# Optimization experiments

Measured on AMD Instinct MI355X. Metric: run time of the kernel, lower is better.

Reference implementation:

```python
import jax, jax.numpy as jnp
import numpy as np

E = 8
DIMS = [512, 1024, 1024, 512]
BATCH = 2048


def _init_w(key, shape):
    a = np.sqrt(6.0 / (shape[-2] * shape[-1]))
    return jax.random.uniform(key, shape, dtype=jnp.float32, minval=-a, maxval=a)


def setup_inputs() -> dict:
    key = jax.random.key(0)
    ks = jax.random.split(key, 8)
    inp = {
        "weight_blend": jax.random.uniform(ks[0], (BATCH, E), dtype=jnp.float32),
        "x": jax.random.normal(ks[1], (BATCH, DIMS[0]), dtype=jnp.float32),
    }
    for i in range(3):
        inp[f"W{i}"] = _init_w(ks[2 + i], (E, DIMS[i + 1], DIMS[i]))
        inp[f"B{i}"] = jnp.zeros((E, DIMS[i + 1], 1), dtype=jnp.float32)
    return inp


def reference(weight_blend, x, W0, B0, W1, B1, W2, B2):
    Ws = [W0, W1, W2]
    Bs = [B0, B1, B2]
    acts = [jax.nn.elu, jax.nn.elu, None]
    for W, B, act in zip(Ws, Bs, acts):
        # dropout p=0 -> identity
        # blended-expert GEMM: sum_e wb[b,e] * (W[e] @ x[b]) == einsum
        t = jnp.einsum("be,eoi,bi->bo", weight_blend, W, x)
        bias = jnp.einsum("be,eo->bo", weight_blend, B[..., 0])
        x = t + bias
        if act is not None:
            x = act(x)
    return x
```

## Files before the change

### kernel.cpp

```cpp
#include <hip/hip_runtime.h>
#include <math.h>

typedef __attribute__((ext_vector_type(8))) short bf16x8;
typedef __attribute__((ext_vector_type(4))) float f32x4;

#define NEXP 8
#define BATCH 2048

__device__ __forceinline__ unsigned short f2bf(float f) {
    union { float f; unsigned u; } v; v.f = f;
    unsigned r = v.u + 0x7FFFu + ((v.u >> 16) & 1u);
    return (unsigned short)(r >> 16);
}

__device__ __forceinline__ float elu_fast(float v) {
    return v > 0.f ? v : (exp2f(v * 1.4426950408889634f) - 1.0f);
}

__device__ __forceinline__ void gl_lds(const char* g, char* l) {
    __builtin_amdgcn_global_load_lds(
        (const __attribute__((address_space(1))) void*)g,
        (__attribute__((address_space(3))) void*)l, 16, 0, 0);
}

__global__ __launch_bounds__(256) void pack_all(
    const float* __restrict__ W0, const float* __restrict__ W1,
    const float* __restrict__ W2, const float* __restrict__ x,
    unsigned short* __restrict__ W0p, unsigned short* __restrict__ W1p,
    unsigned short* __restrict__ W2p, unsigned short* __restrict__ x0p)
{
    __shared__ float T[128 * 36];
    const int bid = blockIdx.x, t = threadIdx.x;

    if (bid < 10240) {
        const float* W; unsigned short* out; int KB, Din, Dout, U, lin;
        if (bid < 2048)      { W = W0; out = W0p; KB = 16; Din = 512;  Dout = 1024; U = 4; lin = bid; }
        else if (bid < 6144) { W = W1; out = W1p; KB = 32; Din = 1024; Dout = 1024; U = 4; lin = bid - 2048; }
        else                 { W = W2; out = W2p; KB = 32; Din = 1024; Dout = 512;  U = 2; lin = bid - 6144; }
        const int e  = lin & 7;
        const int r  = lin >> 3;
        const int kb = r % KB;
        const int nb = r / KB;
        const int N0 = nb * 16 * U;
        const int K0 = kb * 32;
        for (int it = 0; it < U / 2; ++it) {
            const int idx = t + 256 * it;
            const int nl = idx >> 3, k4 = (idx & 7) * 4;
            float4 v = *(const float4*)(W + ((size_t)e * Dout + N0 + nl) * Din + K0 + k4);
            *(float4*)(T + nl * 36 + k4) = v;
        }
        __syncthreads();
        if (t < 64 * U) {
            const int u = t >> 6, l = t & 63;
            const float* p = T + (u * 16 + (l & 15)) * 36 + (l >> 4) * 8;
            bf16x8 h;
            #pragma unroll
            for (int j = 0; j < 8; ++j) h[j] = (short)f2bf(p[j]);
            *(bf16x8*)(out + (size_t)lin * (U * 512) + t * 8) = h;
        }
    } else {
        const int lin = bid - 10240;
        const int kb = lin & 15, mb = lin >> 4;
        for (int it = 0; it < 4; ++it) {
            const int idx = t + 256 * it;
            const int ml = idx >> 3, k4 = (idx & 7) * 4;
            float4 v = *(const float4*)(x + (size_t)(mb * 128 + ml) * 512 + kb * 32 + k4);
            *(float4*)(T + ml * 36 + k4) = v;
        }
        __syncthreads();
        #pragma unroll
        for (int it = 0; it < 2; ++it) {
            const int s = t + 256 * it;
            const int g = s >> 6, l = s & 63;
            const float* p = T + (g * 16 + (l & 15)) * 36 + (l >> 4) * 8;
            bf16x8 h;
            #pragma unroll
            for (int j = 0; j < 8; ++j) h[j] = (short)f2bf(p[j]);
            *(bf16x8*)(x0p + (size_t)lin * 4096 + s * 8) = h;
        }
    }
}

template<int UP>
__device__ __forceinline__ void moe_stage(
    char* smem, int bx, int by,
    const unsigned short* __restrict__ Xp,
    const unsigned short* __restrict__ Wp,
    const float* __restrict__ Bias,
    const float* __restrict__ WBl,
    unsigned short* __restrict__ Yout,
    int KB, int Dout, int KBn)
{
    constexpr int PSTR = 68;
    constexpr unsigned BUFB = 40 * 1024;

    const int tid  = threadIdx.x;
    const int wv   = tid >> 6;
    const int mh   = wv >> 2;
    const int ew   = wv & 3;
    const int l    = tid & 63;
    const int lh   = l >> 4;
    const int ll   = l & 15;
    const int e0   = 2 * ew;
    const int m0   = by * 128 + mh * 64;
    const int n0   = bx * 64;
    const int mb   = by;

    f32x4 acc0[4][4], acc1[4][4];
    #pragma unroll
    for (int t = 0; t < 4; ++t)
        #pragma unroll
        for (int u = 0; u < 4; ++u)
            #pragma unroll
            for (int i = 0; i < 4; ++i) { acc0[t][u][i] = 0.f; acc1[t][u][i] = 0.f; }

    const char* xc = (const char*)Xp;
    const char* wc = (const char*)Wp;
    const int fidbase = wv * 5;
    const char* gp[5]; unsigned kst[5];
    #pragma unroll
    for (int s = 0; s < 5; ++s) {
        const int fid = fidbase + s;
        if (fid < 8) {
            gp[s]  = xc + (unsigned)(mb * KB) * 8192u + (unsigned)fid * 1024u + l * 16u;
            kst[s] = 8192u;
        } else {
            const int idx = fid - 8;
            const int e   = 2 * (idx >> 3) + ((idx >> 2) & 1);
            const int u   = idx & 3;
            const int fn  = bx * 4 + u;
            const int nb  = fn / UP;
            const int uu  = fn % UP;
            gp[s]  = wc + (unsigned)((nb * KB * 8 + e) * UP + uu) * 1024u + l * 16u;
            kst[s] = UP * 8192u;
        }
    }

    auto STAGE = [&](int b, int kk) {
        char* lb = smem + (unsigned)b * BUFB + (unsigned)fidbase * 1024u;
        #pragma unroll
        for (int s = 0; s < 5; ++s)
            gl_lds(gp[s] + (unsigned)kk * kst[s], lb + s * 1024);
    };

    auto COMPUTE = [&](int b) {
        const char* sb = smem + (unsigned)b * BUFB;
        bf16x8 aR[4], b0R[4], b1R[4];
        #pragma unroll
        for (int t = 0; t < 4; ++t)
            aR[t] = *(const bf16x8*)(sb + (mh * 4 + t) * 1024 + l * 16);
        #pragma unroll
        for (int u = 0; u < 4; ++u) {
            b0R[u] = *(const bf16x8*)(sb + (8 + ew * 8 + u) * 1024 + l * 16);
            b1R[u] = *(const bf16x8*)(sb + (8 + ew * 8 + 4 + u) * 1024 + l * 16);
        }
        __builtin_amdgcn_s_setprio(1);
        #pragma unroll
        for (int u = 0; u < 4; ++u)
            #pragma unroll
            for (int t = 0; t < 4; ++t) {
                acc0[t][u] = __builtin_amdgcn_mfma_f32_16x16x32_bf16(aR[t], b0R[u], acc0[t][u], 0, 0, 0);
                acc1[t][u] = __builtin_amdgcn_mfma_f32_16x16x32_bf16(aR[t], b1R[u], acc1[t][u], 0, 0, 0);
            }
        __builtin_amdgcn_s_setprio(0);
    };

    STAGE(0, 0);
    __syncthreads();
    for (int kk = 0; kk < KB; ++kk) {
        if (kk + 1 < KB) STAGE((kk + 1) & 1, kk + 1);
        COMPUTE(kk & 1);
        __syncthreads();
    }

    float* epi = (float*)smem;
    float bi0[4], bi1[4];
    #pragma unroll
    for (int u = 0; u < 4; ++u) {
        const int n = n0 + u * 16 + ll;
        bi0[u] = Bias[(size_t)e0 * Dout + n];
        bi1[u] = Bias[(size_t)(e0 + 1) * Dout + n];
    }
    float2 wbp[4][4];
    #pragma unroll
    for (int t = 0; t < 4; ++t)
        #pragma unroll
        for (int r = 0; r < 4; ++r) {
            const int lm = 16 * t + 4 * lh + r;
            wbp[t][r] = ((const float2*)(WBl + (size_t)(m0 + lm) * NEXP))[ew];
        }

    float* pb = epi + ew * (64 * PSTR);
    #pragma unroll
    for (int h = 0; h < 2; ++h) {
        if (mh == h) {
            #pragma unroll
            for (int t = 0; t < 4; ++t)
                #pragma unroll
                for (int r = 0; r < 4; ++r) {
                    const int lm = 16 * t + 4 * lh + r;
                    #pragma unroll
                    for (int u = 0; u < 4; ++u)
                        pb[lm * PSTR + u * 16 + ll] =
                            wbp[t][r].x * (acc0[t][u][r] + bi0[u]) + wbp[t][r].y * (acc1[t][u][r] + bi1[u]);
                }
        }
        __syncthreads();
        {
            const int kbh = wv >> 2;
            const int g   = wv & 3;
            const int rb  = (g * 16 + ll) * PSTR + kbh * 32 + lh * 8;
            bf16x8 hx;
            #pragma unroll
            for (int j = 0; j < 8; ++j) {
                float v = epi[0 * 64 * PSTR + rb + j]
                        + epi[1 * 64 * PSTR + rb + j]
                        + epi[2 * 64 * PSTR + rb + j]
                        + epi[3 * 64 * PSTR + rb + j];
                v = elu_fast(v);
                hx[j] = (short)f2bf(v);
            }
            unsigned short* dst = Yout +
                ((size_t)(mb * KBn + bx * 2 + kbh) * 8 + h * 4 + g) * 512 + l * 8;
            *(bf16x8*)dst = hx;
        }
        if (h == 0) __syncthreads();
    }
}

template<int UP, int NU>
__device__ __forceinline__ void moe_body(
    float* lds_f, int bx, int by,
    const unsigned short* __restrict__ Xp,
    const unsigned short* __restrict__ Wp,
    const float* __restrict__ Bias,
    const float* __restrict__ WBl,
    void* __restrict__ Yout,
    int KB, int Dout, int KBn, int act, int packed_out)
{
    constexpr int PSTR = NU * 16 + 4;

    const int tid  = threadIdx.x;
    const int ew   = tid >> 6;
    const int l    = tid & 63;
    const int lh   = l >> 4;
    const int ll   = l & 15;
    const int e0   = 2 * ew;
    const int m0   = by * 64;
    const int n0   = bx * (NU * 16);
    const int mb   = by >> 1;
    const int half = by & 1;

    f32x4 acc0[4][NU], acc1[4][NU];
    #pragma unroll
    for (int t = 0; t < 4; ++t)
        #pragma unroll
        for (int u = 0; u < NU; ++u)
            #pragma unroll
            for (int i = 0; i < 4; ++i) { acc0[t][u][i] = 0.f; acc1[t][u][i] = 0.f; }

    unsigned aoff[4];
    #pragma unroll
    for (int t = 0; t < 4; ++t)
        aoff[t] = (unsigned)(mb * KB) * 8192u + (unsigned)(half * 4 + t) * 1024u + l * 16u;
    unsigned boff0[NU], boff1[NU];
    #pragma unroll
    for (int u = 0; u < NU; ++u) {
        const int fn = bx * NU + u;
        const int nb = fn / UP;
        const int uu = fn % UP;
        boff0[u] = (((unsigned)(nb * KB) * 8 + e0) * UP + uu) * 1024u + l * 16u;
        boff1[u] = boff0[u] + UP * 1024u;
    }
    const unsigned astr = 8192u;
    const unsigned bstr = UP * 8192u;
    const char* xc = (const char*)Xp;
    const char* wc = (const char*)Wp;

    bf16x8 aR[2][4], b0R[2][NU], b1R[2][NU];

    auto LOAD = [&](int s, int kk) {
        const unsigned ab = (unsigned)kk * astr;
        const unsigned bb = (unsigned)kk * bstr;
        #pragma unroll
        for (int t = 0; t < 4; ++t)
            aR[s][t] = *(const bf16x8*)(xc + aoff[t] + ab);
        #pragma unroll
        for (int u = 0; u < NU; ++u) {
            b0R[s][u] = *(const bf16x8*)(wc + boff0[u] + bb);
            b1R[s][u] = *(const bf16x8*)(wc + boff1[u] + bb);
        }
    };
    auto MF = [&](int s) {
        __builtin_amdgcn_s_setprio(1);
        #pragma unroll
        for (int u = 0; u < NU; ++u)
            #pragma unroll
            for (int t = 0; t < 4; ++t) {
                acc0[t][u] = __builtin_amdgcn_mfma_f32_16x16x32_bf16(aR[s][t], b0R[s][u], acc0[t][u], 0, 0, 0);
                acc1[t][u] = __builtin_amdgcn_mfma_f32_16x16x32_bf16(aR[s][t], b1R[s][u], acc1[t][u], 0, 0, 0);
            }
        __builtin_amdgcn_s_setprio(0);
    };

    LOAD(0, 0);
    for (int kk = 0; kk < KB; kk += 2) {
        if (kk + 1 < KB) LOAD(1, kk + 1);
        MF(0);
        if (kk + 2 < KB) LOAD(0, kk + 2);
        MF(1);
    }

    float bi0[NU], bi1[NU];
    #pragma unroll
    for (int u = 0; u < NU; ++u) {
        const int n = n0 + u * 16 + ll;
        bi0[u] = Bias[(size_t)e0 * Dout + n];
        bi1[u] = Bias[(size_t)(e0 + 1) * Dout + n];
    }
    float2 wbp[4][4];
    #pragma unroll
    for (int t = 0; t < 4; ++t)
        #pragma unroll
        for (int r = 0; r < 4; ++r) {
            const int lm = 16 * t + 4 * lh + r;
            wbp[t][r] = ((const float2*)(WBl + (size_t)(m0 + lm) * NEXP))[ew];
        }

    float* pb = lds_f + ew * (64 * PSTR);
    #pragma unroll
    for (int t = 0; t < 4; ++t)
        #pragma unroll
        for (int r = 0; r < 4; ++r) {
            const int lm = 16 * t + 4 * lh + r;
            #pragma unroll
            for (int u = 0; u < NU; ++u)
                pb[lm * PSTR + u * 16 + ll] =
                    wbp[t][r].x * (acc0[t][u][r] + bi0[u]) + wbp[t][r].y * (acc1[t][u][r] + bi1[u]);
        }
    __syncthreads();

    if (packed_out) {
        if constexpr (NU == 4) {
            #pragma unroll
            for (int it = 0; it < 2; ++it) {
                const int kbh = it;
                const int g   = tid >> 6;
                const int le  = tid & 63;
                const int lhh = le >> 4, lle = le & 15;
                const int rb  = (g * 16 + lle) * PSTR + kbh * 32 + lhh * 8;
                bf16x8 h;
                #pragma unroll
                for (int j = 0; j < 8; ++j) {
                    float v = lds_f[0 * 64 * PSTR + rb + j]
                            + lds_f[1 * 64 * PSTR + rb + j]
                            + lds_f[2 * 64 * PSTR + rb + j]
                            + lds_f[3 * 64 * PSTR + rb + j];
                    if (act) v = elu_fast(v);
                    h[j] = (short)f2bf(v);
                }
                unsigned short* dst = (unsigned short*)Yout +
                    ((size_t)(mb * KBn + bx * 2 + kbh) * 8 + half * 4 + g) * 512 + le * 8;
                *(bf16x8*)dst = h;
            }
        }
    } else {
        constexpr int F4R = NU * 4;
        #pragma unroll
        for (int it = 0; it < NU; ++it) {
            const int idx = tid + 256 * it;
            const int row = idx / F4R;
            const int c4  = (idx % F4R) * 4;
            const int rb  = row * PSTR + c4;
            float4 s  = *(const float4*)(lds_f + 0 * 64 * PSTR + rb);
            float4 q1 = *(const float4*)(lds_f + 1 * 64 * PSTR + rb);
            float4 q2 = *(const float4*)(lds_f + 2 * 64 * PSTR + rb);
            float4 q3 = *(const float4*)(lds_f + 3 * 64 * PSTR + rb);
            s.x += q1.x + q2.x + q3.x;
            s.y += q1.y + q2.y + q3.y;
            s.z += q1.z + q2.z + q3.z;
            s.w += q1.w + q2.w + q3.w;
            if (act) {
                s.x = elu_fast(s.x);
                s.y = elu_fast(s.y);
                s.z = elu_fast(s.z);
                s.w = elu_fast(s.w);
            }
            *(float4*)((float*)Yout + (size_t)(m0 + row) * Dout + n0 + c4) = s;
        }
    }
}

__device__ __forceinline__ void swz256(int& bx, int& by) {
    const int bid = blockIdx.x;
    const int xcd = bid & 7;
    const int loc = bid >> 3;
    bx = xcd * 2 + (loc & 1);
    by = loc >> 1;
}
__device__ __forceinline__ void swz_pair(int& bx, int& by) {
    const int bid = blockIdx.x;
    const int xcd = bid & 7;
    const int loc = bid >> 3;
    bx = xcd * 2 + (loc & 1);
    by = loc >> 1;
}

__global__ __launch_bounds__(512, 2) void moe_l0(
    const unsigned short* __restrict__ Xp, const unsigned short* __restrict__ Wp,
    const float* __restrict__ Bias, const float* __restrict__ WBl,
    unsigned short* __restrict__ Yout, int KB, int Dout, int KBn)
{
    __shared__ __align__(16) char smem[2 * 40 * 1024];
    int bx, by; swz256(bx, by);
    moe_stage<4>(smem, bx, by, Xp, Wp, Bias, WBl, Yout, KB, Dout, KBn);
}
__global__ __launch_bounds__(512, 2) void moe_l1(
    const unsigned short* __restrict__ Xp, const unsigned short* __restrict__ Wp,
    const float* __restrict__ Bias, const float* __restrict__ WBl,
    unsigned short* __restrict__ Yout, int KB, int Dout, int KBn)
{
    __shared__ __align__(16) char smem[2 * 40 * 1024];
    int bx, by; swz256(bx, by);
    moe_stage<4>(smem, bx, by, Xp, Wp, Bias, WBl, Yout, KB, Dout, KBn);
}
__global__ __launch_bounds__(256, 2) void moe_l2(
    const unsigned short* __restrict__ Xp, const unsigned short* __restrict__ Wp,
    const float* __restrict__ Bias, const float* __restrict__ WBl,
    void* __restrict__ Yout, int KB, int Dout, int KBn, int act, int packed_out)
{
    __shared__ __align__(16) float lds_f[4 * 64 * 36];
    int bx, by; swz_pair(bx, by);
    moe_body<2, 2>(lds_f, bx, by, Xp, Wp, Bias, WBl, Yout, KB, Dout, KBn, act, packed_out);
}

#define BM 64
#define BNF 64
#define BKF 16
#define PAD 4

__global__ __launch_bounds__(256) void moe_layer_f32(
    const float* __restrict__ X, const float* __restrict__ W,
    const float* __restrict__ Bias, const float* __restrict__ WB,
    float* __restrict__ Y, int Din, int Dout, int act)
{
    __shared__ float As[BKF][BM + PAD];
    __shared__ float Bs[BKF][BNF + PAD];
    const int tid = threadIdx.x;
    const int tm = tid >> 4, tn = tid & 15;
    const int m0 = blockIdx.y * BM, n0 = blockIdx.x * BNF;
    const int lr = tid >> 2, lc = (tid & 3) << 2;
    float acc[4][4] = {};
    const float* xrow  = X  + (size_t)(m0 + lr) * Din;
    const float* wbrow = WB + (size_t)(m0 + lr) * NEXP;
    const float* wrow0 = W  + (size_t)(n0 + lr) * Din;
    for (int e = 0; e < NEXP; ++e) {
        const float wbe = wbrow[e];
        const float* wrow = wrow0 + (size_t)e * Dout * Din;
        for (int k0 = 0; k0 < Din; k0 += BKF) {
            float4 av = *(const float4*)(xrow + k0 + lc);
            float4 bv = *(const float4*)(wrow + k0 + lc);
            __syncthreads();
            As[lc+0][lr] = av.x*wbe; As[lc+1][lr] = av.y*wbe;
            As[lc+2][lr] = av.z*wbe; As[lc+3][lr] = av.w*wbe;
            Bs[lc+0][lr] = bv.x; Bs[lc+1][lr] = bv.y;
            Bs[lc+2][lr] = bv.z; Bs[lc+3][lr] = bv.w;
            __syncthreads();
            #pragma unroll
            for (int k = 0; k < BKF; ++k) {
                float4 a = *(const float4*)&As[k][tm << 2];
                float4 b = *(const float4*)&Bs[k][tn << 2];
                acc[0][0]+=a.x*b.x; acc[0][1]+=a.x*b.y; acc[0][2]+=a.x*b.z; acc[0][3]+=a.x*b.w;
                acc[1][0]+=a.y*b.x; acc[1][1]+=a.y*b.y; acc[1][2]+=a.y*b.z; acc[1][3]+=a.y*b.w;
                acc[2][0]+=a.z*b.x; acc[2][1]+=a.z*b.y; acc[2][2]+=a.z*b.z; acc[2][3]+=a.z*b.w;
                acc[3][0]+=a.w*b.x; acc[3][1]+=a.w*b.y; acc[3][2]+=a.w*b.z; acc[3][3]+=a.w*b.w;
            }
        }
    }
    #pragma unroll
    for (int im = 0; im < 4; ++im) {
        const int m = m0 + (tm << 2) + im;
        const float* wbm = WB + (size_t)m * NEXP;
        float wv[NEXP];
        #pragma unroll
        for (int e = 0; e < NEXP; ++e) wv[e] = wbm[e];
        #pragma unroll
        for (int in = 0; in < 4; ++in) {
            const int n = n0 + (tn << 2) + in;
            float bsum = 0.f;
            #pragma unroll
            for (int e = 0; e < NEXP; ++e) bsum += wv[e] * Bias[(size_t)e * Dout + n];
            float v = acc[im][in] + bsum;
            if (act) v = v > 0.f ? v : expm1f(v);
            acc[im][in] = v;
        }
        float4 o = make_float4(acc[im][0], acc[im][1], acc[im][2], acc[im][3]);
        *(float4*)(Y + (size_t)m * Dout + n0 + (tn << 2)) = o;
    }
}

extern "C" void kernel_launch(void* const* d_in, const int* in_sizes, int n_in,
                              void* d_out, int out_size, void* d_ws, size_t ws_size,
                              hipStream_t stream)
{
    (void)in_sizes; (void)n_in; (void)out_size;
    const float* wb = (const float*)d_in[0];
    const float* x  = (const float*)d_in[1];
    const float* W0 = (const float*)d_in[2];
    const float* B0 = (const float*)d_in[3];
    const float* W1 = (const float*)d_in[4];
    const float* B1 = (const float*)d_in[5];
    const float* W2 = (const float*)d_in[6];
    const float* B2 = (const float*)d_in[7];
    float* out = (float*)d_out;

    const size_t NW0 = (size_t)8*1024*512, NW1 = (size_t)8*1024*1024, NW2 = (size_t)8*512*1024;
    const size_t NX0 = (size_t)BATCH*512, NX1 = (size_t)BATCH*1024;
    const size_t need = (NW0 + NW1 + NW2 + NX0 + 2 * NX1) * 2;

    if (ws_size >= need) {
        unsigned short* W0p = (unsigned short*)d_ws;
        unsigned short* W1p = W0p + NW0;
        unsigned short* W2p = W1p + NW1;
        unsigned short* x0p = W2p + NW2;
        unsigned short* x1p = x0p + NX0;
        unsigned short* x2p = x1p + NX1;
        pack_all<<<10496, 256, 0, stream>>>(W0, W1, W2, x, W0p, W1p, W2p, x0p);
        moe_l0<<<256, 512, 0, stream>>>(x0p, W0p, B0, wb, x1p, 16, 1024, 32);
        moe_l1<<<256, 512, 0, stream>>>(x1p, W1p, B1, wb, x2p, 32, 1024, 32);
        moe_l2<<<512, 256, 0, stream>>>(x2p, W2p, B2, wb, out, 32, 512,  0, 0, 0);
    } else {
        float* x1 = (float*)d_ws;
        float* x2 = x1 + (size_t)BATCH * 1024;
        moe_layer_f32<<<dim3(1024/BNF, BATCH/BM), 256, 0, stream>>>(x,  W0, B0, wb, x1, 512,  1024, 1);
        moe_layer_f32<<<dim3(1024/BNF, BATCH/BM), 256, 0, stream>>>(x1, W1, B1, wb, x2, 1024, 1024, 1);
        moe_layer_f32<<<dim3(512/BNF,  BATCH/BM), 256, 0, stream>>>(x2, W2, B2, wb, out, 1024, 512,  0);
    }
}
```

Before: 186.9 us.

## Stage layer-2 operands through LDS with async global-to-LDS double buffering

```diff
diff --git a/kernel.cpp b/kernel.cpp
--- a/kernel.cpp
+++ b/kernel.cpp
@@ -228,17 +228,18 @@
     }
 }
 
-template<int UP, int NU>
-__device__ __forceinline__ void moe_body(
-    float* lds_f, int bx, int by,
+__device__ __forceinline__ void moe_stage_l2(
+    char* smem, int bx, int by,
     const unsigned short* __restrict__ Xp,
     const unsigned short* __restrict__ Wp,
     const float* __restrict__ Bias,
     const float* __restrict__ WBl,
-    void* __restrict__ Yout,
-    int KB, int Dout, int KBn, int act, int packed_out)
-{
-    constexpr int PSTR = NU * 16 + 4;
+    float* __restrict__ Yout,
+    int KB, int Dout)
+{
+    constexpr int UP = 2;
+    constexpr int PSTR = 36;
+    constexpr unsigned BUFB = 20 * 1024;
 
     const int tid  = threadIdx.x;
     const int ew   = tid >> 6;
@@ -247,73 +248,81 @@
     const int ll   = l & 15;
     const int e0   = 2 * ew;
     const int m0   = by * 64;
-    const int n0   = bx * (NU * 16);
+    const int n0   = bx * 32;
     const int mb   = by >> 1;
     const int half = by & 1;
 
-    f32x4 acc0[4][NU], acc1[4][NU];
+    f32x4 acc0[4][2], acc1[4][2];
     #pragma unroll
     for (int t = 0; t < 4; ++t)
         #pragma unroll
-        for (int u = 0; u < NU; ++u)
+        for (int u = 0; u < 2; ++u)
             #pragma unroll
             for (int i = 0; i < 4; ++i) { acc0[t][u][i] = 0.f; acc1[t][u][i] = 0.f; }
 
-    unsigned aoff[4];
-    #pragma unroll
-    for (int t = 0; t < 4; ++t)
-        aoff[t] = (unsigned)(mb * KB) * 8192u + (unsigned)(half * 4 + t) * 1024u + l * 16u;
-    unsigned boff0[NU], boff1[NU];
-    #pragma unroll
-    for (int u = 0; u < NU; ++u) {
-        const int fn = bx * NU + u;
-        const int nb = fn / UP;
-        const int uu = fn % UP;
-        boff0[u] = (((unsigned)(nb * KB) * 8 + e0) * UP + uu) * 1024u + l * 16u;
-        boff1[u] = boff0[u] + UP * 1024u;
-    }
-    const unsigned astr = 8192u;
-    const unsigned bstr = UP * 8192u;
     const char* xc = (const char*)Xp;
     const char* wc = (const char*)Wp;
-
-    bf16x8 aR[2][4], b0R[2][NU], b1R[2][NU];
-
-    auto LOAD = [&](int s, int kk) {
-        const unsigned ab = (unsigned)kk * astr;
-        const unsigned bb = (unsigned)kk * bstr;
+    const int fidbase = ew * 5;
+    const char* gp[5]; unsigned kst[5];
+    #pragma unroll
+    for (int s = 0; s < 5; ++s) {
+        const int fid = fidbase + s;
+        if (fid < 4) {
+            gp[s]  = xc + (unsigned)(mb * KB) * 8192u + (unsigned)(half * 4 + fid) * 1024u + l * 16u;
+            kst[s] = 8192u;
+        } else {
+            const int idx = fid - 4;
+            const int e   = idx >> 1;
+            const int u   = idx & 1;
+            const int fn  = bx * 2 + u;
+            const int nb  = fn / UP;
+            const int uu  = fn % UP;
+            gp[s]  = wc + (unsigned)((nb * KB * 8 + e) * UP + uu) * 1024u + l * 16u;
+            kst[s] = UP * 8192u;
+        }
+    }
+
+    auto STAGE = [&](int b, int kk) {
+        char* lb = smem + (unsigned)b * BUFB + (unsigned)fidbase * 1024u;
+        #pragma unroll
+        for (int s = 0; s < 5; ++s)
+            gl_lds(gp[s] + (unsigned)kk * kst[s], lb + s * 1024);
+    };
+
+    auto COMPUTE = [&](int b) {
+        const char* sb = smem + (unsigned)b * BUFB;
+        bf16x8 aR[4], b0R[2], b1R[2];
         #pragma unroll
         for (int t = 0; t < 4; ++t)
-            aR[s][t] = *(const bf16x8*)(xc + aoff[t] + ab);
-        #pragma unroll
-        for (int u = 0; u < NU; ++u) {
-            b0R[s][u] = *(const bf16x8*)(wc + boff0[u] + bb);
-            b1R[s][u] = *(const bf16x8*)(wc + boff1[u] + bb);
-        }
-    };
-    auto MF = [&](int s) {
+            aR[t] = *(const bf16x8*)(sb + t * 1024 + l * 16);
+        #pragma unroll
+        for (int u = 0; u < 2; ++u) {
+            b0R[u] = *(const bf16x8*)(sb + (4 + e0 * 2 + u) * 1024 + l * 16);
+            b1R[u] = *(const bf16x8*)(sb + (4 + (e0 + 1) * 2 + u) * 1024 + l * 16);
+        }
         __builtin_amdgcn_s_setprio(1);
         #pragma unroll
-        for (int u = 0; u < NU; ++u)
+        for (int u = 0; u < 2; ++u)
             #pragma unroll
             for (int t = 0; t < 4; ++t) {
-                acc0[t][u] = __builtin_amdgcn_mfma_f32_16x16x32_bf16(aR[s][t], b0R[s][u], acc0[t][u], 0, 0, 0);
-                acc1[t][u] = __builtin_amdgcn_mfma_f32_16x16x32_bf16(aR[s][t], b1R[s][u], acc1[t][u], 0, 0, 0);
+                acc0[t][u] = __builtin_amdgcn_mfma_f32_16x16x32_bf16(aR[t], b0R[u], acc0[t][u], 0, 0, 0);
+                acc1[t][u] = __builtin_amdgcn_mfma_f32_16x16x32_bf16(aR[t], b1R[u], acc1[t][u], 0, 0, 0);
             }
         __builtin_amdgcn_s_setprio(0);
     };
 
-    LOAD(0, 0);
-    for (int kk = 0; kk < KB; kk += 2) {
-        if (kk + 1 < KB) LOAD(1, kk + 1);
-        MF(0);
-        if (kk + 2 < KB) LOAD(0, kk + 2);
-        MF(1);
-    }
-
-    float bi0[NU], bi1[NU];
-    #pragma unroll
-    for (int u = 0; u < NU; ++u) {
+    STAGE(0, 0);
+    __syncthreads();
+    for (int kk = 0; kk < KB; ++kk) {
+        if (kk + 1 < KB) STAGE((kk + 1) & 1, kk + 1);
+        COMPUTE(kk & 1);
+        __syncthreads();
+    }
+
+    float* epi = (float*)smem;
+    float bi0[2], bi1[2];
+    #pragma unroll
+    for (int u = 0; u < 2; ++u) {
         const int n = n0 + u * 16 + ll;
         bi0[u] = Bias[(size_t)e0 * Dout + n];
         bi1[u] = Bias[(size_t)(e0 + 1) * Dout + n];
@@ -327,67 +336,34 @@
             wbp[t][r] = ((const float2*)(WBl + (size_t)(m0 + lm) * NEXP))[ew];
         }
 
-    float* pb = lds_f + ew * (64 * PSTR);
+    float* pb = epi + ew * (64 * PSTR);
     #pragma unroll
     for (int t = 0; t < 4; ++t)
         #pragma unroll
         for (int r = 0; r < 4; ++r) {
             const int lm = 16 * t + 4 * lh + r;
             #pragma unroll
-            for (int u = 0; u < NU; ++u)
+            for (int u = 0; u < 2; ++u)
                 pb[lm * PSTR + u * 16 + ll] =
                     wbp[t][r].x * (acc0[t][u][r] + bi0[u]) + wbp[t][r].y * (acc1[t][u][r] + bi1[u]);
         }
     __syncthreads();
 
-    if (packed_out) {
-        if constexpr (NU == 4) {
-            #pragma unroll
-            for (int it = 0; it < 2; ++it) {
-                const int kbh = it;
-                const int g   = tid >> 6;
-                const int le  = tid & 63;
-                const int lhh = le >> 4, lle = le & 15;
-                const int rb  = (g * 16 + lle) * PSTR + kbh * 32 + lhh * 8;
-                bf16x8 h;
-                #pragma unroll
-                for (int j = 0; j < 8; ++j) {
-                    float v = lds_f[0 * 64 * PSTR + rb + j]
-                            + lds_f[1 * 64 * PSTR + rb + j]
-                            + lds_f[2 * 64 * PSTR + rb + j]
-                            + lds_f[3 * 64 * PSTR + rb + j];
-                    if (act) v = elu_fast(v);
-                    h[j] = (short)f2bf(v);
-                }
-                unsigned short* dst = (unsigned short*)Yout +
-                    ((size_t)(mb * KBn + bx * 2 + kbh) * 8 + half * 4 + g) * 512 + le * 8;
-                *(bf16x8*)dst = h;
-            }
-        }
-    } else {
-        constexpr int F4R = NU * 4;
-        #pragma unroll
-        for (int it = 0; it < NU; ++it) {
-            const int idx = tid + 256 * it;
-            const int row = idx / F4R;
-            const int c4  = (idx % F4R) * 4;
-            const int rb  = row * PSTR + c4;
-            float4 s  = *(const float4*)(lds_f + 0 * 64 * PSTR + rb);
-            float4 q1 = *(const float4*)(lds_f + 1 * 64 * PSTR + rb);
-            float4 q2 = *(const float4*)(lds_f + 2 * 64 * PSTR + rb);
-            float4 q3 = *(const float4*)(lds_f + 3 * 64 * PSTR + rb);
-            s.x += q1.x + q2.x + q3.x;
-            s.y += q1.y + q2.y + q3.y;
-            s.z += q1.z + q2.z + q3.z;
-            s.w += q1.w + q2.w + q3.w;
-            if (act) {
-                s.x = elu_fast(s.x);
-                s.y = elu_fast(s.y);
-                s.z = elu_fast(s.z);
-                s.w = elu_fast(s.w);
-            }
-            *(float4*)((float*)Yout + (size_t)(m0 + row) * Dout + n0 + c4) = s;
-        }
+    #pragma unroll
+    for (int it = 0; it < 2; ++it) {
+        const int idx = tid + 256 * it;
+        const int row = idx >> 3;
+        const int c4  = (idx & 7) * 4;
+        const int rb  = row * PSTR + c4;
+        float4 s  = *(const float4*)(epi + 0 * 64 * PSTR + rb);
+        float4 q1 = *(const float4*)(epi + 1 * 64 * PSTR + rb);
+        float4 q2 = *(const float4*)(epi + 2 * 64 * PSTR + rb);
+        float4 q3 = *(const float4*)(epi + 3 * 64 * PSTR + rb);
+        s.x += q1.x + q2.x + q3.x;
+        s.y += q1.y + q2.y + q3.y;
+        s.z += q1.z + q2.z + q3.z;
+        s.w += q1.w + q2.w + q3.w;
+        *(float4*)(Yout + (size_t)(m0 + row) * Dout + n0 + c4) = s;
     }
 }
 
@@ -427,11 +403,11 @@
 __global__ __launch_bounds__(256, 2) void moe_l2(
     const unsigned short* __restrict__ Xp, const unsigned short* __restrict__ Wp,
     const float* __restrict__ Bias, const float* __restrict__ WBl,
-    void* __restrict__ Yout, int KB, int Dout, int KBn, int act, int packed_out)
-{
-    __shared__ __align__(16) float lds_f[4 * 64 * 36];
+    float* __restrict__ Yout, int KB, int Dout)
+{
+    __shared__ __align__(16) char smem[2 * 20 * 1024];
     int bx, by; swz_pair(bx, by);
-    moe_body<2, 2>(lds_f, bx, by, Xp, Wp, Bias, WBl, Yout, KB, Dout, KBn, act, packed_out);
+    moe_stage_l2(smem, bx, by, Xp, Wp, Bias, WBl, Yout, KB, Dout);
 }
 
 #define BM 64
@@ -528,7 +504,7 @@
         pack_all<<<10496, 256, 0, stream>>>(W0, W1, W2, x, W0p, W1p, W2p, x0p);
         moe_l0<<<256, 512, 0, stream>>>(x0p, W0p, B0, wb, x1p, 16, 1024, 32);
         moe_l1<<<256, 512, 0, stream>>>(x1p, W1p, B1, wb, x2p, 32, 1024, 32);
-        moe_l2<<<512, 256, 0, stream>>>(x2p, W2p, B2, wb, out, 32, 512,  0, 0, 0);
+        moe_l2<<<512, 256, 0, stream>>>(x2p, W2p, B2, wb, out, 32, 512);
     } else {
         float* x1 = (float*)d_ws;
         float* x2 = x1 + (size_t)BATCH * 1024;
```

New measurement: 186.7 us (median of 2 runs). About the same (-0.1%).
